# Kernel optimization log

Measured on AMD Instinct MI355X. Metric: run time of the kernel, lower is better.

The kernel has to match this reference:

```python
import jax, jax.numpy as jnp
import numpy as np

DIM = 4096
K = 16  # 2**bits, bits=4
SCALE = 1.0 / DIM ** 0.5
# Lloyd-Max optimal 16-level quantizer centroids for N(0,1)
LLOYD_MAX_4BIT = np.array([
    -2.7326, -2.0690, -1.6181, -1.2562, -0.9424, -0.6568, -0.3881, -0.1284,
     0.1284,  0.3881,  0.6568,  0.9424,  1.2562,  1.6181,  2.0690,  2.7326,
], dtype=np.float32)


def setup_inputs() -> dict:
    key = jax.random.key(0)
    k_x, k_q = jax.random.split(key)
    x = jax.random.normal(k_x, (2048, DIM), dtype=jnp.float32)
    # Random orthogonal rotation via QR, matching torch.linalg.qr(randn(dim, dim))
    g = jax.random.normal(k_q, (DIM, DIM), dtype=jnp.float32)
    rotation, _ = jnp.linalg.qr(g)
    codebook = jnp.asarray(LLOYD_MAX_4BIT)
    return {"x": x, "rotation": rotation, "codebook": codebook}


def reference(x, rotation, codebook):
    # x: (N, dim); rotation: (dim, dim) orthogonal; codebook: (K,)
    shape = x.shape
    x_flat = x.reshape(-1, DIM).astype(jnp.float32)
    y = x_flat @ rotation.T                      # (N, dim) rotate
    y_norm = y / SCALE                           # coords ~ N(0, 1)
    # (N, dim, K) distance tensor -> argmin over codebook axis
    dists = jnp.abs(y_norm[..., None] - codebook)
    idx = jnp.argmin(dists, axis=-1)             # (N, dim) int32
    y_hat = codebook[idx] * SCALE                # gather + rescale
    x_hat = y_hat @ rotation                     # inverse rotation
    return x_hat.reshape(shape)
```

## Files before the change

### kernel.cpp

```cpp
#include <hip/hip_runtime.h>
#include <hip/hip_bf16.h>


typedef __attribute__((ext_vector_type(8))) _Float16 f16x8;
typedef __attribute__((ext_vector_type(4))) float f32x4;

__device__ __forceinline__ unsigned short f2h(float f) {
    _Float16 h = (_Float16)f;
    return *reinterpret_cast<unsigned short*>(&h);
}

__global__ __launch_bounds__(256) void convert_x_kernel(
    const float* __restrict__ x, unsigned short* __restrict__ xb) {
    const int i = (blockIdx.x * 256 + threadIdx.x) * 4;
    float4 v = *reinterpret_cast<const float4*>(x + i);
    ushort4 b;
    b.x = f2h(v.x); b.y = f2h(v.y); b.z = f2h(v.z); b.w = f2h(v.w);
    *reinterpret_cast<ushort4*>(xb + i) = b;
}

__global__ __launch_bounds__(256) void conv_rot_kernel(
    const float* __restrict__ R, unsigned short* __restrict__ Rb,
    unsigned short* __restrict__ Rt) {
    __shared__ float t[64][65];
    const int tid = threadIdx.x;
    const int tr = blockIdx.y * 64, tc = blockIdx.x * 64;
    const int r0 = tid >> 4;
    const int c4 = (tid & 15) << 2;
#pragma unroll
    for (int i = 0; i < 4; i++) {
        const int r = r0 + i * 16;
        float4 v = *reinterpret_cast<const float4*>(
            &R[(size_t)(tr + r) * 4096 + tc + c4]);
        ushort4 b;
        b.x = f2h(v.x); b.y = f2h(v.y); b.z = f2h(v.z); b.w = f2h(v.w);
        *reinterpret_cast<ushort4*>(&Rb[(size_t)(tr + r) * 4096 + tc + c4]) = b;
        t[r][c4 + 0] = v.x; t[r][c4 + 1] = v.y;
        t[r][c4 + 2] = v.z; t[r][c4 + 3] = v.w;
    }
    __syncthreads();
#pragma unroll
    for (int i = 0; i < 16; i++) {
        const int idx = tid + 256 * i;
        const int rr = idx >> 6;
        const int cc = idx & 63;
        Rt[(size_t)(tc + rr) * 4096 + tr + cc] = f2h(t[cc][rr]);
    }
}

constexpr int GK = 4096;
constexpr int BM = 128, BN = 256, BK = 64;
constexpr int NT = GK / BK;
constexpr int A_BYTES = BM * BK * 2;
constexpr int BUF_BYTES = (BM + BN) * BK * 2;
constexpr int LDS_DYN = 3 * BUF_BYTES;

template <bool QUANT>
__global__ __launch_bounds__(512, 2) void gemm_nt_kernel(
    const unsigned short* __restrict__ A, const unsigned short* __restrict__ Bt,
    void* __restrict__ Cout, const float* __restrict__ cb16) {
    extern __shared__ char smem[];
    const int tid = threadIdx.x;
    const int lane = tid & 63;
    const int w = tid >> 6;
    const int wm = w >> 2;
    const int wn = w & 3;

    const int bid = blockIdx.x;
    const int wgid = (bid & 7) * 32 + (bid >> 3);
    const int tn = wgid & 15;
    const int tm = wgid >> 4;

    f32x4 acc[4][4];
#pragma unroll
    for (int m = 0; m < 4; m++)
#pragma unroll
        for (int n = 0; n < 4; n++) acc[m][n] = (f32x4){0.f, 0.f, 0.f, 0.f};

    const int srow = tid >> 3;
    const int scol = (((tid & 7) ^ (srow & 7)) << 3);
    const size_t arow0 = (size_t)(tm * BM) * GK;
    const size_t brow0 = (size_t)(tn * BN) * GK;
    const int wbase = (w << 10);

    auto stage = [&](int tile, int chunk) {
        const int b = tile % 3;
        const int k0 = tile * BK;
        const unsigned short* src;
        int ldsoff;
        if (chunk < 2) {
            src = A + arow0 + (size_t)(chunk * 64 + srow) * GK + k0 + scol;
            ldsoff = b * BUF_BYTES + chunk * 8192 + wbase;
        } else {
            src = Bt + brow0 + (size_t)((chunk - 2) * 64 + srow) * GK + k0 + scol;
            ldsoff = b * BUF_BYTES + A_BYTES + (chunk - 2) * 8192 + wbase;
        }
        __builtin_amdgcn_global_load_lds(
            (const __attribute__((address_space(1))) void*)src,
            (__attribute__((address_space(3))) void*)(smem + ldsoff), 16, 0, 0);
    };

    const int arow = (wm * 64 + (lane & 15)) * 128;
    const int brow = A_BYTES + (wn * 64 + (lane & 15)) * 128;
    const int slotx = lane >> 4;
    const int sw0 = ((slotx ^ (lane & 7)) << 4);
    const int sw1 = (((4 + slotx) ^ (lane & 7)) << 4);

#define LDA(m, sw) (*reinterpret_cast<const f16x8*>(smem + lb + arow + (m) * 2048 + (sw)))
#define LDB(n, sw) (*reinterpret_cast<const f16x8*>(smem + lb + brow + (n) * 2048 + (sw)))
#define MFMA_ROW(aR, r)                                                          \
    acc[r][0] = __builtin_amdgcn_mfma_f32_16x16x32_f16(aR, b0, acc[r][0], 0, 0, 0); \
    acc[r][1] = __builtin_amdgcn_mfma_f32_16x16x32_f16(aR, b1, acc[r][1], 0, 0, 0); \
    acc[r][2] = __builtin_amdgcn_mfma_f32_16x16x32_f16(aR, b2, acc[r][2], 0, 0, 0); \
    acc[r][3] = __builtin_amdgcn_mfma_f32_16x16x32_f16(aR, b3, acc[r][3], 0, 0, 0);
#define PH_SYNC                                        \
    __builtin_amdgcn_s_barrier();                      \
    asm volatile("s_waitcnt lgkmcnt(0)" ::: "memory"); \
    __builtin_amdgcn_sched_barrier(0);

    stage(0, 0); stage(0, 1); stage(0, 2); stage(0, 3); stage(0, 4); stage(0, 5);
    stage(1, 0); stage(1, 1);
    asm volatile("s_waitcnt vmcnt(2)" ::: "memory");
    __builtin_amdgcn_s_barrier();
    __builtin_amdgcn_sched_barrier(0);

    int lb = 0;
    for (int t = 0; t < NT; ++t) {
        f16x8 a0, a1, a2, a3, b0, b1, b2, b3;
        a0 = LDA(0, sw0); a1 = LDA(1, sw0); a2 = LDA(2, sw0); a3 = LDA(3, sw0);
        b0 = LDB(0, sw0); b1 = LDB(1, sw0); b2 = LDB(2, sw0); b3 = LDB(3, sw0);
        if (t + 1 < NT) { stage(t + 1, 2); stage(t + 1, 3);
                          stage(t + 1, 4); stage(t + 1, 5); }
        PH_SYNC
        __builtin_amdgcn_s_setprio(1);
        MFMA_ROW(a0, 0) MFMA_ROW(a1, 1) MFMA_ROW(a2, 2) MFMA_ROW(a3, 3)
        __builtin_amdgcn_s_setprio(0);
        __builtin_amdgcn_s_barrier();
        a0 = LDA(0, sw1); a1 = LDA(1, sw1); a2 = LDA(2, sw1); a3 = LDA(3, sw1);
        b0 = LDB(0, sw1); b1 = LDB(1, sw1); b2 = LDB(2, sw1); b3 = LDB(3, sw1);
        if (t + 2 < NT) { stage(t + 2, 0); stage(t + 2, 1); }
        PH_SYNC
        __builtin_amdgcn_s_setprio(1);
        MFMA_ROW(a0, 0) MFMA_ROW(a1, 1) MFMA_ROW(a2, 2) MFMA_ROW(a3, 3)
        __builtin_amdgcn_s_setprio(0);
        if (t + 1 < NT) {
            if (t + 2 < NT) {
                asm volatile("s_waitcnt vmcnt(2)" ::: "memory");
            } else {
                asm volatile("s_waitcnt vmcnt(0)" ::: "memory");
            }
            __builtin_amdgcn_s_barrier();
            __builtin_amdgcn_sched_barrier(0);
        }
        lb = (lb == 2 * BUF_BYTES) ? 0 : lb + BUF_BYTES;
    }
#undef LDA
#undef LDB
#undef MFMA_ROW
#undef PH_SYNC

    const int crow0 = tm * BM + wm * 64 + ((lane >> 4) << 2);
    const int ccol0 = tn * BN + wn * 64 + (lane & 15);
    if constexpr (QUANT) {
        float c[16];
#pragma unroll
        for (int i = 0; i < 16; i++) c[i] = cb16[i];
        unsigned short* O = (unsigned short*)Cout;
#pragma unroll
        for (int m = 0; m < 4; m++)
#pragma unroll
            for (int n = 0; n < 4; n++)
#pragma unroll
                for (int j = 0; j < 4; j++) {
                    const float yn = acc[m][n][j] * 64.0f;
                    float v = c[0];
#pragma unroll
                    for (int i = 0; i < 15; i++) {
                        const float bnd = 0.5f * (c[i] + c[i + 1]);
                        v = (yn > bnd) ? c[i + 1] : v;
                    }
                    O[(size_t)(crow0 + m * 16 + j) * 4096 + ccol0 + n * 16] =
                        f2h(v * 0.015625f);
                }
    } else {
        float* O = (float*)Cout;
#pragma unroll
        for (int m = 0; m < 4; m++)
#pragma unroll
            for (int n = 0; n < 4; n++)
#pragma unroll
                for (int j = 0; j < 4; j++)
                    O[(size_t)(crow0 + m * 16 + j) * 4096 + ccol0 + n * 16] =
                        acc[m][n][j];
    }
}

extern "C" void kernel_launch(void* const* d_in, const int* in_sizes, int n_in,
                              void* d_out, int out_size, void* d_ws,
                              size_t ws_size, hipStream_t stream) {
    const float* x = (const float*)d_in[0];
    const float* rot = (const float*)d_in[1];
    const float* cb = (const float*)d_in[2];
    float* out = (float*)d_out;

    unsigned short* Xh = (unsigned short*)d_ws;
    unsigned short* Rh = Xh + (size_t)2048 * 4096;
    unsigned short* Rt = Rh + (size_t)4096 * 4096;
    unsigned short* Yh = Rt + (size_t)4096 * 4096;

    (void)hipFuncSetAttribute(
        reinterpret_cast<const void*>(&gemm_nt_kernel<true>),
        hipFuncAttributeMaxDynamicSharedMemorySize, LDS_DYN);
    (void)hipFuncSetAttribute(
        reinterpret_cast<const void*>(&gemm_nt_kernel<false>),
        hipFuncAttributeMaxDynamicSharedMemorySize, LDS_DYN);

    convert_x_kernel<<<8192, 256, 0, stream>>>(x, Xh);
    conv_rot_kernel<<<dim3(64, 64), 256, 0, stream>>>(rot, Rh, Rt);
    gemm_nt_kernel<true><<<256, 512, LDS_DYN, stream>>>(Xh, Rh, (void*)Yh, cb);
    gemm_nt_kernel<false><<<256, 512, LDS_DYN, stream>>>(Yh, Rt, (void*)out, nullptr);
}
```

Baseline: 172.4 us.

## Load GEMM A operand directly into registers, stage only B through LDS

```diff
diff --git a/kernel.cpp b/kernel.cpp
--- a/kernel.cpp
+++ b/kernel.cpp
@@ -51,9 +51,8 @@
 constexpr int GK = 4096;
 constexpr int BM = 128, BN = 256, BK = 64;
 constexpr int NT = GK / BK;
-constexpr int A_BYTES = BM * BK * 2;
-constexpr int BUF_BYTES = (BM + BN) * BK * 2;
-constexpr int LDS_DYN = 3 * BUF_BYTES;
+constexpr int BUF = BN * BK * 2;
+constexpr int LDS_DYN = 3 * BUF;
 
 template <bool QUANT>
 __global__ __launch_bounds__(512, 2) void gemm_nt_kernel(
@@ -77,36 +76,43 @@
 #pragma unroll
         for (int n = 0; n < 4; n++) acc[m][n] = (f32x4){0.f, 0.f, 0.f, 0.f};
 
+    const unsigned short* Ap0 = A +
+        (size_t)(tm * BM + wm * 64 + 0 * 16 + (lane & 15)) * GK + ((lane >> 4) << 3);
+    const unsigned short* Ap1 = Ap0 + (size_t)16 * GK;
+    const unsigned short* Ap2 = Ap0 + (size_t)32 * GK;
+    const unsigned short* Ap3 = Ap0 + (size_t)48 * GK;
+
     const int srow = tid >> 3;
     const int scol = (((tid & 7) ^ (srow & 7)) << 3);
-    const size_t arow0 = (size_t)(tm * BM) * GK;
-    const size_t brow0 = (size_t)(tn * BN) * GK;
+    const unsigned short* Bp0 = Bt +
+        (size_t)(tn * BN + 0 * 64 + srow) * GK + scol;
+    const unsigned short* Bp1 = Bp0 + (size_t)64 * GK;
+    const unsigned short* Bp2 = Bp0 + (size_t)128 * GK;
+    const unsigned short* Bp3 = Bp0 + (size_t)192 * GK;
     const int wbase = (w << 10);
 
-    auto stage = [&](int tile, int chunk) {
-        const int b = tile % 3;
-        const int k0 = tile * BK;
-        const unsigned short* src;
-        int ldsoff;
-        if (chunk < 2) {
-            src = A + arow0 + (size_t)(chunk * 64 + srow) * GK + k0 + scol;
-            ldsoff = b * BUF_BYTES + chunk * 8192 + wbase;
-        } else {
-            src = Bt + brow0 + (size_t)((chunk - 2) * 64 + srow) * GK + k0 + scol;
-            ldsoff = b * BUF_BYTES + A_BYTES + (chunk - 2) * 8192 + wbase;
-        }
-        __builtin_amdgcn_global_load_lds(
-            (const __attribute__((address_space(1))) void*)src,
-            (__attribute__((address_space(3))) void*)(smem + ldsoff), 16, 0, 0);
-    };
-
-    const int arow = (wm * 64 + (lane & 15)) * 128;
-    const int brow = A_BYTES + (wn * 64 + (lane & 15)) * 128;
+#define STAGE_B(dstbase)                                                       \
+    {                                                                          \
+        __builtin_amdgcn_global_load_lds(                                      \
+            (const __attribute__((address_space(1))) void*)Bp0,                \
+            (__attribute__((address_space(3))) void*)(smem + (dstbase) + 0 * 8192 + wbase), 16, 0, 0); \
+        __builtin_amdgcn_global_load_lds(                                      \
+            (const __attribute__((address_space(1))) void*)Bp1,                \
+            (__attribute__((address_space(3))) void*)(smem + (dstbase) + 1 * 8192 + wbase), 16, 0, 0); \
+        __builtin_amdgcn_global_load_lds(                                      \
+            (const __attribute__((address_space(1))) void*)Bp2,                \
+            (__attribute__((address_space(3))) void*)(smem + (dstbase) + 2 * 8192 + wbase), 16, 0, 0); \
+        __builtin_amdgcn_global_load_lds(                                      \
+            (const __attribute__((address_space(1))) void*)Bp3,                \
+            (__attribute__((address_space(3))) void*)(smem + (dstbase) + 3 * 8192 + wbase), 16, 0, 0); \
+        Bp0 += BK; Bp1 += BK; Bp2 += BK; Bp3 += BK;                            \
+    }
+
+    const int brow = (wn * 64 + (lane & 15)) * 128;
     const int slotx = lane >> 4;
     const int sw0 = ((slotx ^ (lane & 7)) << 4);
     const int sw1 = (((4 + slotx) ^ (lane & 7)) << 4);
 
-#define LDA(m, sw) (*reinterpret_cast<const f16x8*>(smem + lb + arow + (m) * 2048 + (sw)))
 #define LDB(n, sw) (*reinterpret_cast<const f16x8*>(smem + lb + brow + (n) * 2048 + (sw)))
 #define MFMA_ROW(aR, r)                                                          \
     acc[r][0] = __builtin_amdgcn_mfma_f32_16x16x32_f16(aR, b0, acc[r][0], 0, 0, 0); \
@@ -118,43 +124,71 @@
     asm volatile("s_waitcnt lgkmcnt(0)" ::: "memory"); \
     __builtin_amdgcn_sched_barrier(0);
 
-    stage(0, 0); stage(0, 1); stage(0, 2); stage(0, 3); stage(0, 4); stage(0, 5);
-    stage(1, 0); stage(1, 1);
-    asm volatile("s_waitcnt vmcnt(2)" ::: "memory");
+    f16x8 aA0, aA1, aA2, aA3, aA4, aA5, aA6, aA7;
+    f16x8 aB0, aB1, aB2, aB3, aB4, aB5, aB6, aB7;
+
+#define LOAD_A(AN)                                              \
+    {                                                           \
+        AN##0 = *reinterpret_cast<const f16x8*>(Ap0);           \
+        AN##1 = *reinterpret_cast<const f16x8*>(Ap0 + 32);      \
+        AN##2 = *reinterpret_cast<const f16x8*>(Ap1);           \
+        AN##3 = *reinterpret_cast<const f16x8*>(Ap1 + 32);      \
+        AN##4 = *reinterpret_cast<const f16x8*>(Ap2);           \
+        AN##5 = *reinterpret_cast<const f16x8*>(Ap2 + 32);      \
+        AN##6 = *reinterpret_cast<const f16x8*>(Ap3);           \
+        AN##7 = *reinterpret_cast<const f16x8*>(Ap3 + 32);      \
+        Ap0 += BK; Ap1 += BK; Ap2 += BK; Ap3 += BK;             \
+    }
+
+    STAGE_B(0)
+    LOAD_A(aA)
+    STAGE_B(BUF)
+    asm volatile("s_waitcnt vmcnt(4)" ::: "memory");
     __builtin_amdgcn_s_barrier();
     __builtin_amdgcn_sched_barrier(0);
 
     int lb = 0;
-    for (int t = 0; t < NT; ++t) {
-        f16x8 a0, a1, a2, a3, b0, b1, b2, b3;
-        a0 = LDA(0, sw0); a1 = LDA(1, sw0); a2 = LDA(2, sw0); a3 = LDA(3, sw0);
-        b0 = LDB(0, sw0); b1 = LDB(1, sw0); b2 = LDB(2, sw0); b3 = LDB(3, sw0);
-        if (t + 1 < NT) { stage(t + 1, 2); stage(t + 1, 3);
-                          stage(t + 1, 4); stage(t + 1, 5); }
-        PH_SYNC
-        __builtin_amdgcn_s_setprio(1);
-        MFMA_ROW(a0, 0) MFMA_ROW(a1, 1) MFMA_ROW(a2, 2) MFMA_ROW(a3, 3)
-        __builtin_amdgcn_s_setprio(0);
-        __builtin_amdgcn_s_barrier();
-        a0 = LDA(0, sw1); a1 = LDA(1, sw1); a2 = LDA(2, sw1); a3 = LDA(3, sw1);
-        b0 = LDB(0, sw1); b1 = LDB(1, sw1); b2 = LDB(2, sw1); b3 = LDB(3, sw1);
-        if (t + 2 < NT) { stage(t + 2, 0); stage(t + 2, 1); }
-        PH_SYNC
-        __builtin_amdgcn_s_setprio(1);
-        MFMA_ROW(a0, 0) MFMA_ROW(a1, 1) MFMA_ROW(a2, 2) MFMA_ROW(a3, 3)
-        __builtin_amdgcn_s_setprio(0);
-        if (t + 1 < NT) {
-            if (t + 2 < NT) {
-                asm volatile("s_waitcnt vmcnt(2)" ::: "memory");
-            } else {
-                asm volatile("s_waitcnt vmcnt(0)" ::: "memory");
-            }
-            __builtin_amdgcn_s_barrier();
-            __builtin_amdgcn_sched_barrier(0);
-        }
-        lb = (lb == 2 * BUF_BYTES) ? 0 : lb + BUF_BYTES;
-    }
-#undef LDA
+    int wb = 2 * BUF;
+
+#define TILE_BODY(AC, AN, t)                                                   \
+    {                                                                          \
+        f16x8 b0, b1, b2, b3;                                                  \
+                                                            \
+        b0 = LDB(0, sw0); b1 = LDB(1, sw0); b2 = LDB(2, sw0); b3 = LDB(3, sw0);\
+        if ((t) + 1 < NT) LOAD_A(AN)                                           \
+        PH_SYNC                                                                \
+        __builtin_amdgcn_s_setprio(1);                                         \
+        MFMA_ROW(AC##0, 0) MFMA_ROW(AC##2, 1) MFMA_ROW(AC##4, 2) MFMA_ROW(AC##6, 3) \
+        __builtin_amdgcn_s_setprio(0);                                         \
+        __builtin_amdgcn_s_barrier();                                          \
+                                                            \
+        b0 = LDB(0, sw1); b1 = LDB(1, sw1); b2 = LDB(2, sw1); b3 = LDB(3, sw1);\
+        if ((t) + 2 < NT) STAGE_B(wb)                                          \
+        PH_SYNC                                                                \
+        __builtin_amdgcn_s_setprio(1);                                         \
+        MFMA_ROW(AC##1, 0) MFMA_ROW(AC##3, 1) MFMA_ROW(AC##5, 2) MFMA_ROW(AC##7, 3) \
+        __builtin_amdgcn_s_setprio(0);                                         \
+                     \
+        if ((t) + 1 < NT) {                                                    \
+            if ((t) + 2 < NT) {                                                \
+                asm volatile("s_waitcnt vmcnt(4)" ::: "memory");               \
+            } else {                                                           \
+                asm volatile("s_waitcnt vmcnt(0)" ::: "memory");               \
+            }                                                                  \
+            __builtin_amdgcn_s_barrier();                                      \
+            __builtin_amdgcn_sched_barrier(0);                                 \
+            lb = (lb == 2 * BUF) ? 0 : lb + BUF;                               \
+            wb = (wb == 2 * BUF) ? 0 : wb + BUF;                               \
+        }                                                                      \
+    }
+
+    for (int t = 0; t < NT; t += 2) {
+        TILE_BODY(aA, aB, t)
+        TILE_BODY(aB, aA, t + 1)
+    }
+#undef TILE_BODY
+#undef LOAD_A
+#undef STAGE_B
 #undef LDB
 #undef MFMA_ROW
 #undef PH_SYNC
```

Result: slower. 355.3 us (+106.1%).

## Halve GEMM K-tile to 32 and restructure pipeline for higher occupancy

Applied to the files above, without the earlier changes.

```diff
diff --git a/kernel.cpp b/kernel.cpp
--- a/kernel.cpp
+++ b/kernel.cpp
@@ -49,14 +49,14 @@
 }
 
 constexpr int GK = 4096;
-constexpr int BM = 128, BN = 256, BK = 64;
+constexpr int BM = 128, BN = 256, BK = 32;
 constexpr int NT = GK / BK;
-constexpr int A_BYTES = BM * BK * 2;
-constexpr int BUF_BYTES = (BM + BN) * BK * 2;
-constexpr int LDS_DYN = 3 * BUF_BYTES;
+constexpr int A_LDS = BM * BK * 2;
+constexpr int BUF = (BM + BN) * BK * 2;
+constexpr int LDS_DYN = 3 * BUF;
 
 template <bool QUANT>
-__global__ __launch_bounds__(512, 2) void gemm_nt_kernel(
+__global__ __launch_bounds__(512, 4) void gemm_nt_kernel(
     const unsigned short* __restrict__ A, const unsigned short* __restrict__ Bt,
     void* __restrict__ Cout, const float* __restrict__ cb16) {
     extern __shared__ char smem[];
@@ -77,87 +77,73 @@
 #pragma unroll
         for (int n = 0; n < 4; n++) acc[m][n] = (f32x4){0.f, 0.f, 0.f, 0.f};
 
-    const int srow = tid >> 3;
-    const int scol = (((tid & 7) ^ (srow & 7)) << 3);
-    const size_t arow0 = (size_t)(tm * BM) * GK;
-    const size_t brow0 = (size_t)(tn * BN) * GK;
+    const int srow = tid >> 2;
+    const int scol = (((tid & 3) ^ ((srow >> 1) & 3)) << 3);
+    const unsigned short* ApS = A + (size_t)(tm * BM + srow) * GK + scol;
+    const unsigned short* BpS0 = Bt + (size_t)(tn * BN + srow) * GK + scol;
+    const unsigned short* BpS1 = BpS0 + (size_t)128 * GK;
     const int wbase = (w << 10);
 
-    auto stage = [&](int tile, int chunk) {
-        const int b = tile % 3;
-        const int k0 = tile * BK;
-        const unsigned short* src;
-        int ldsoff;
-        if (chunk < 2) {
-            src = A + arow0 + (size_t)(chunk * 64 + srow) * GK + k0 + scol;
-            ldsoff = b * BUF_BYTES + chunk * 8192 + wbase;
-        } else {
-            src = Bt + brow0 + (size_t)((chunk - 2) * 64 + srow) * GK + k0 + scol;
-            ldsoff = b * BUF_BYTES + A_BYTES + (chunk - 2) * 8192 + wbase;
-        }
-        __builtin_amdgcn_global_load_lds(
-            (const __attribute__((address_space(1))) void*)src,
-            (__attribute__((address_space(3))) void*)(smem + ldsoff), 16, 0, 0);
-    };
-
-    const int arow = (wm * 64 + (lane & 15)) * 128;
-    const int brow = A_BYTES + (wn * 64 + (lane & 15)) * 128;
-    const int slotx = lane >> 4;
-    const int sw0 = ((slotx ^ (lane & 7)) << 4);
-    const int sw1 = (((4 + slotx) ^ (lane & 7)) << 4);
-
-#define LDA(m, sw) (*reinterpret_cast<const f16x8*>(smem + lb + arow + (m) * 2048 + (sw)))
-#define LDB(n, sw) (*reinterpret_cast<const f16x8*>(smem + lb + brow + (n) * 2048 + (sw)))
+#define STAGE(dstbase)                                                         \
+    {                                                                          \
+        __builtin_amdgcn_global_load_lds(                                      \
+            (const __attribute__((address_space(1))) void*)ApS,                \
+            (__attribute__((address_space(3))) void*)(smem + (dstbase) + wbase), 16, 0, 0); \
+        __builtin_amdgcn_global_load_lds(                                      \
+            (const __attribute__((address_space(1))) void*)BpS0,               \
+            (__attribute__((address_space(3))) void*)(smem + (dstbase) + A_LDS + wbase), 16, 0, 0); \
+        __builtin_amdgcn_global_load_lds(                                      \
+            (const __attribute__((address_space(1))) void*)BpS1,               \
+            (__attribute__((address_space(3))) void*)(smem + (dstbase) + A_LDS + 8192 + wbase), 16, 0, 0); \
+        ApS += BK; BpS0 += BK; BpS1 += BK;                                     \
+    }
+
+    const int sw = (((lane >> 4) ^ (((lane & 15) >> 1) & 3)) << 4);
+    const int arow = (wm * 64 + (lane & 15)) * 64;
+    const int brow = A_LDS + (wn * 64 + (lane & 15)) * 64;
+
+#define LDA(m) (*reinterpret_cast<const f16x8*>(smem + lb + arow + (m) * 1024 + sw))
+#define LDB(n) (*reinterpret_cast<const f16x8*>(smem + lb + brow + (n) * 1024 + sw))
 #define MFMA_ROW(aR, r)                                                          \
     acc[r][0] = __builtin_amdgcn_mfma_f32_16x16x32_f16(aR, b0, acc[r][0], 0, 0, 0); \
     acc[r][1] = __builtin_amdgcn_mfma_f32_16x16x32_f16(aR, b1, acc[r][1], 0, 0, 0); \
     acc[r][2] = __builtin_amdgcn_mfma_f32_16x16x32_f16(aR, b2, acc[r][2], 0, 0, 0); \
     acc[r][3] = __builtin_amdgcn_mfma_f32_16x16x32_f16(aR, b3, acc[r][3], 0, 0, 0);
-#define PH_SYNC                                        \
-    __builtin_amdgcn_s_barrier();                      \
-    asm volatile("s_waitcnt lgkmcnt(0)" ::: "memory"); \
-    __builtin_amdgcn_sched_barrier(0);
-
-    stage(0, 0); stage(0, 1); stage(0, 2); stage(0, 3); stage(0, 4); stage(0, 5);
-    stage(1, 0); stage(1, 1);
-    asm volatile("s_waitcnt vmcnt(2)" ::: "memory");
+
+    STAGE(0)
+    STAGE(BUF)
+    asm volatile("s_waitcnt vmcnt(3)" ::: "memory");
     __builtin_amdgcn_s_barrier();
     __builtin_amdgcn_sched_barrier(0);
 
     int lb = 0;
+    int wb = 2 * BUF;
     for (int t = 0; t < NT; ++t) {
         f16x8 a0, a1, a2, a3, b0, b1, b2, b3;
-        a0 = LDA(0, sw0); a1 = LDA(1, sw0); a2 = LDA(2, sw0); a3 = LDA(3, sw0);
-        b0 = LDB(0, sw0); b1 = LDB(1, sw0); b2 = LDB(2, sw0); b3 = LDB(3, sw0);
-        if (t + 1 < NT) { stage(t + 1, 2); stage(t + 1, 3);
-                          stage(t + 1, 4); stage(t + 1, 5); }
-        PH_SYNC
-        __builtin_amdgcn_s_setprio(1);
-        MFMA_ROW(a0, 0) MFMA_ROW(a1, 1) MFMA_ROW(a2, 2) MFMA_ROW(a3, 3)
-        __builtin_amdgcn_s_setprio(0);
-        __builtin_amdgcn_s_barrier();
-        a0 = LDA(0, sw1); a1 = LDA(1, sw1); a2 = LDA(2, sw1); a3 = LDA(3, sw1);
-        b0 = LDB(0, sw1); b1 = LDB(1, sw1); b2 = LDB(2, sw1); b3 = LDB(3, sw1);
-        if (t + 2 < NT) { stage(t + 2, 0); stage(t + 2, 1); }
-        PH_SYNC
+        a0 = LDA(0); a1 = LDA(1); a2 = LDA(2); a3 = LDA(3);
+        b0 = LDB(0); b1 = LDB(1); b2 = LDB(2); b3 = LDB(3);
+        if (t + 2 < NT) STAGE(wb)
+        asm volatile("s_waitcnt lgkmcnt(0)" ::: "memory");
+        __builtin_amdgcn_sched_barrier(0);
         __builtin_amdgcn_s_setprio(1);
         MFMA_ROW(a0, 0) MFMA_ROW(a1, 1) MFMA_ROW(a2, 2) MFMA_ROW(a3, 3)
         __builtin_amdgcn_s_setprio(0);
         if (t + 1 < NT) {
             if (t + 2 < NT) {
-                asm volatile("s_waitcnt vmcnt(2)" ::: "memory");
+                asm volatile("s_waitcnt vmcnt(3)" ::: "memory");
             } else {
                 asm volatile("s_waitcnt vmcnt(0)" ::: "memory");
             }
             __builtin_amdgcn_s_barrier();
             __builtin_amdgcn_sched_barrier(0);
+            lb = (lb == 2 * BUF) ? 0 : lb + BUF;
+            wb = (wb == 2 * BUF) ? 0 : wb + BUF;
         }
-        lb = (lb == 2 * BUF_BYTES) ? 0 : lb + BUF_BYTES;
     }
 #undef LDA
 #undef LDB
 #undef MFMA_ROW
-#undef PH_SYNC
+#undef STAGE
 
     const int crow0 = tm * BM + wm * 64 + ((lane >> 4) << 2);
     const int ccol0 = tn * BN + wn * 64 + (lane & 15);
```

Result: slower. 176.4 us (+2.3%).
